# Kernel optimization log

Measured on AMD Instinct MI355X. Metric: run time of the kernel, lower is better.

The kernel has to match this reference:

```python
import jax, jax.numpy as jnp
import numpy as np

N, E, F, DE, G, C = 50000, 800000, 64, 32, 512, 2
EPS = 1e-5


def setup_inputs() -> dict:
    key = jax.random.key(0)
    ks = jax.random.split(key, 12)
    Z = 2 * F + DE  # CGConv concat dim [x_i, x_j, edge_attr]
    inp = {
        "x": jax.random.normal(ks[0], (N, F), dtype=jnp.float32),
        "edge_index": jax.random.randint(ks[1], (2, E), 0, N, dtype=jnp.int32),
        "edge_attr": jax.random.normal(ks[2], (E, DE), dtype=jnp.float32),
        "batch": jnp.sort(jax.random.randint(ks[3], (N,), 0, G, dtype=jnp.int32)),
        # CGConv lin_f / lin_s : (2F+De) -> F, with bias
        "Wf": jax.random.normal(ks[4], (Z, F), dtype=jnp.float32) * 0.05,
        "bf": jnp.zeros((F,), dtype=jnp.float32),
        "Ws": jax.random.normal(ks[5], (Z, F), dtype=jnp.float32) * 0.05,
        "bs": jnp.zeros((F,), dtype=jnp.float32),
        # CGConv internal BatchNorm (training-mode batch stats)
        "bn_w": jnp.ones((F,), dtype=jnp.float32),
        "bn_b": jnp.zeros((F,), dtype=jnp.float32),
        # PyG LayerNorm (graph mode, batch=None -> whole-tensor stats)
        "ln_w": jnp.ones((F,), dtype=jnp.float32),
        "ln_b": jnp.zeros((F,), dtype=jnp.float32),
        # final linear (2F -> C) and output LayerNorm
        "Wl": jax.random.normal(ks[6], (2 * F, C), dtype=jnp.float32) * 0.05,
        "bl": jnp.zeros((C,), dtype=jnp.float32),
        "ln4_w": jnp.ones((C,), dtype=jnp.float32),
        "ln4_b": jnp.zeros((C,), dtype=jnp.float32),
    }
    return inp


def _pyg_layernorm(x, w, b):
    # torch_geometric.nn.LayerNorm, mode='graph', batch=None: whole-tensor stats
    xc = x - jnp.mean(x)
    out = xc / (jnp.sqrt(jnp.mean(xc * xc)) + EPS)
    return out * w + b


def reference(x, edge_index, edge_attr, batch, Wf, bf, Ws, bs, bn_w, bn_b,
              ln_w, ln_b, Wl, bl, ln4_w, ln4_b):
    src = edge_index[0]  # x_j (source)
    dst = edge_index[1]  # x_i (target / aggregation index)

    # CGConv message: sigmoid(lin_f(z)) * softplus(lin_s(z)), z=[x_i,x_j,e]
    z = jnp.concatenate([x[dst], x[src], edge_attr], axis=1)  # [E, 2F+De]
    msg = jax.nn.sigmoid(z @ Wf + bf) * jax.nn.softplus(z @ Ws + bs)  # [E,F]

    # scatter-add aggregation to target nodes
    agg = jax.ops.segment_sum(msg, dst, num_segments=N)  # [N,F]

    # CGConv batch_norm=True (training-mode batch statistics over nodes)
    mu = jnp.mean(agg, axis=0)
    var = jnp.mean((agg - mu) ** 2, axis=0)
    agg = (agg - mu) / jnp.sqrt(var + EPS) * bn_w + bn_b

    # residual
    h = agg + x

    # LayerNorm + softplus
    h = jax.nn.softplus(_pyg_layernorm(h, ln_w, ln_b))

    # global mean / add pooling over graphs
    add_pool = jax.ops.segment_sum(h, batch, num_segments=G)  # [G,F]
    counts = jax.ops.segment_sum(jnp.ones((N,), h.dtype), batch, num_segments=G)
    mean_pool = add_pool / jnp.maximum(counts, 1.0)[:, None]

    g = jnp.concatenate([mean_pool, add_pool], axis=1)  # [G, 2F]
    out = g @ Wl + bl  # [G, C]
    out = _pyg_layernorm(out, ln4_w, ln4_b)
    return out
```

## Files before the change

### kernel.cpp

```cpp
#include <hip/hip_runtime.h>
#include <math.h>

#define EPSF 1e-5f

typedef short bf16x8 __attribute__((ext_vector_type(8)));
typedef float f32x4 __attribute__((ext_vector_type(4)));

static __device__ __forceinline__ unsigned short f2bf(float x) {
  unsigned u = __float_as_uint(x);
  unsigned r = (u + 0x7FFFu + ((u >> 16) & 1u)) >> 16;
  return (unsigned short)r;
}

union BU { uint4 u; bf16x8 v; };

__global__ __launch_bounds__(512) void bpack_kernel(
    const float* __restrict__ Wf, const float* __restrict__ Ws,
    unsigned short* __restrict__ Bfrag) {
  const int ks = blockIdx.x;
  const int t8 = threadIdx.x >> 6, l = threadIdx.x & 63;
  const int q = l & 15, g = l >> 4;
  const float* W = (t8 < 4) ? Wf : Ws;
  const int col = (t8 & 3) * 16 + q;
  unsigned short out[8];
#pragma unroll
  for (int i = 0; i < 8; ++i) {
    int r = ks * 32 + g * 8 + i;
    int wr = (r < 32) ? (128 + r) : (r - 32);
    out[i] = f2bf(W[(size_t)wr * 64 + col]);
  }
  *(uint4*)&Bfrag[((size_t)(ks * 8 + t8) * 64 + l) * 8] = *(uint4*)out;
}

__global__ void hist_kernel(const int* __restrict__ ei, int* __restrict__ deg,
                            int E) {
  int i = blockIdx.x * blockDim.x + threadIdx.x;
  if (i < E) atomicAdd(&deg[ei[E + i]], 1);
}

__global__ __launch_bounds__(256) void scan_a(const int* __restrict__ deg,
                                              int* __restrict__ bsum, int N) {
  const int idx = blockIdx.x * 256 + threadIdx.x;
  int v = (idx < N) ? deg[idx] : 0;
#pragma unroll
  for (int o = 32; o > 0; o >>= 1) v += __shfl_down(v, o);
  __shared__ int ws4[4];
  if ((threadIdx.x & 63) == 0) ws4[threadIdx.x >> 6] = v;
  __syncthreads();
  if (threadIdx.x == 0) bsum[blockIdx.x] = ws4[0] + ws4[1] + ws4[2] + ws4[3];
}

__global__ __launch_bounds__(256) void scan_b(const int* __restrict__ bsum,
                                              int* __restrict__ bpre, int NB) {
  const int t = threadIdx.x;
  const int lane = t & 63, w = t >> 6;
  int v = (t < NB) ? bsum[t] : 0;
  int sc = v;
#pragma unroll
  for (int o = 1; o < 64; o <<= 1) {
    int u = __shfl_up(sc, o);
    if (lane >= o) sc += u;
  }
  __shared__ int wsum[4];
  if (lane == 63) wsum[w] = sc;
  __syncthreads();
  int add = 0;
#pragma unroll
  for (int k = 0; k < 4; ++k) add += (k < w) ? wsum[k] : 0;
  bpre[t] = (sc - v) + add;
}

__global__ __launch_bounds__(256) void scan_c(const int* __restrict__ deg,
                                              const int* __restrict__ bpre,
                                              int* __restrict__ offsets,
                                              int* __restrict__ cursor, int N) {
  const int t = threadIdx.x;
  const int lane = t & 63, w = t >> 6;
  const int idx = blockIdx.x * 256 + t;
  int d = (idx < N) ? deg[idx] : 0;
  int sc = d;
#pragma unroll
  for (int o = 1; o < 64; o <<= 1) {
    int u = __shfl_up(sc, o);
    if (lane >= o) sc += u;
  }
  __shared__ int wsum[4];
  if (lane == 63) wsum[w] = sc;
  __syncthreads();
  int add = bpre[blockIdx.x];
#pragma unroll
  for (int k = 0; k < 4; ++k) add += (k < w) ? wsum[k] : 0;
  const int off = add + (sc - d);
  if (idx < N) {
    offsets[idx] = off;
    cursor[idx] = off;
    if (idx == N - 1) offsets[N] = off + d;
  }
}

__global__ void scatter_kernel(const int* __restrict__ ei,
                               int* __restrict__ cursor,
                               int4* __restrict__ epair4, int E) {
  int i = blockIdx.x * blockDim.x + threadIdx.x;
  if (i < E) {
    int dst = ei[E + i];
    int pos = atomicAdd(&cursor[dst], 1);
    epair4[pos] = make_int4(i, ei[i], dst, 0);
  }
}

__global__ __launch_bounds__(256) void edge_fused(
    const int4* __restrict__ epair4, const float* __restrict__ eattr,
    const float* __restrict__ x, const unsigned short* __restrict__ Bfrag,
    const float* __restrict__ bfv_, const float* __restrict__ bsv_,
    float* __restrict__ agg, int E, int N) {
  __shared__ __align__(16) unsigned short Ash[5][64][40];
  __shared__ __align__(16) int srcl[64];
  __shared__ __align__(16) int dstl[64];
  __shared__ __align__(16) int eidx[64];
  __shared__ __align__(4) unsigned char ridb[64];

  const int t = threadIdx.x, lane = t & 63, w = t >> 6;
  const int q = lane & 15, g = lane >> 4;
  const int base = blockIdx.x * 64;

  bf16x8 Bf[5], Bs[5];
#pragma unroll
  for (int ks = 0; ks < 5; ++ks) {
    BU u1, u2;
    u1.u = ((const uint4*)Bfrag)[(size_t)((ks * 8 + w) * 64 + lane)];
    u2.u = ((const uint4*)Bfrag)[(size_t)((ks * 8 + w + 4) * 64 + lane)];
    Bf[ks] = u1.v;
    Bs[ks] = u2.v;
  }
  const int feat = w * 16 + q;
  const float bfv = bfv_[feat];
  const float bsv = bsv_[feat];

  if (w == 0) {
    const int eg = base + lane;
    int4 p = make_int4(0, 0, 0x7FFFFFFF, 0);
    if (eg < E) p = epair4[eg];
    eidx[lane] = p.x;
    srcl[lane] = p.y;
    dstl[lane] = p.z;
    int d = p.z;
    int dprev = __shfl_up(d, 1);
    int flag = (lane == 0 || d != dprev) ? 1 : 0;
    int sc = flag;
#pragma unroll
    for (int o = 1; o < 64; o <<= 1) {
      int u = __shfl_up(sc, o);
      if (lane >= o) sc += u;
    }
    ridb[lane] = (unsigned char)(sc - 1);
  }
  __syncthreads();

  {
    const int row = t >> 2, c = t & 3;
    const int ei_ = eidx[row];
    int d_ = dstl[row];
    if (d_ >= N) d_ = 0;
    const int s_ = srcl[row];

    const float* er = eattr + (size_t)ei_ * 32 + c * 8;
    float4 v0 = *(const float4*)er;
    float4 v1 = *(const float4*)(er + 4);
    bf16x8 sv;
    sv[0] = (short)f2bf(v0.x); sv[1] = (short)f2bf(v0.y);
    sv[2] = (short)f2bf(v0.z); sv[3] = (short)f2bf(v0.w);
    sv[4] = (short)f2bf(v1.x); sv[5] = (short)f2bf(v1.y);
    sv[6] = (short)f2bf(v1.z); sv[7] = (short)f2bf(v1.w);
    *(bf16x8*)&Ash[0][row][c * 8] = sv;

    const float* xd = x + (size_t)d_ * 64 + c * 16;
    float4 a0 = *(const float4*)xd;
    float4 a1 = *(const float4*)(xd + 4);
    float4 a2 = *(const float4*)(xd + 8);
    float4 a3 = *(const float4*)(xd + 12);
    bf16x8 s0, s1;
    s0[0] = (short)f2bf(a0.x); s0[1] = (short)f2bf(a0.y);
    s0[2] = (short)f2bf(a0.z); s0[3] = (short)f2bf(a0.w);
    s0[4] = (short)f2bf(a1.x); s0[5] = (short)f2bf(a1.y);
    s0[6] = (short)f2bf(a1.z); s0[7] = (short)f2bf(a1.w);
    s1[0] = (short)f2bf(a2.x); s1[1] = (short)f2bf(a2.y);
    s1[2] = (short)f2bf(a2.z); s1[3] = (short)f2bf(a2.w);
    s1[4] = (short)f2bf(a3.x); s1[5] = (short)f2bf(a3.y);
    s1[6] = (short)f2bf(a3.z); s1[7] = (short)f2bf(a3.w);
    *(bf16x8*)&Ash[1 + (c >> 1)][row][(c & 1) * 16] = s0;
    *(bf16x8*)&Ash[1 + (c >> 1)][row][(c & 1) * 16 + 8] = s1;

    const float* xs = x + (size_t)s_ * 64 + c * 16;
    float4 b0 = *(const float4*)xs;
    float4 b1 = *(const float4*)(xs + 4);
    float4 b2 = *(const float4*)(xs + 8);
    float4 b3 = *(const float4*)(xs + 12);
    bf16x8 t0, t1;
    t0[0] = (short)f2bf(b0.x); t0[1] = (short)f2bf(b0.y);
    t0[2] = (short)f2bf(b0.z); t0[3] = (short)f2bf(b0.w);
    t0[4] = (short)f2bf(b1.x); t0[5] = (short)f2bf(b1.y);
    t0[6] = (short)f2bf(b1.z); t0[7] = (short)f2bf(b1.w);
    t1[0] = (short)f2bf(b2.x); t1[1] = (short)f2bf(b2.y);
    t1[2] = (short)f2bf(b2.z); t1[3] = (short)f2bf(b2.w);
    t1[4] = (short)f2bf(b3.x); t1[5] = (short)f2bf(b3.y);
    t1[6] = (short)f2bf(b3.z); t1[7] = (short)f2bf(b3.w);
    *(bf16x8*)&Ash[3 + (c >> 1)][row][(c & 1) * 16] = t0;
    *(bf16x8*)&Ash[3 + (c >> 1)][row][(c & 1) * 16 + 8] = t1;
  }
  __syncthreads();

  f32x4 accf[4], accs[4];
#pragma unroll
  for (int mt = 0; mt < 4; ++mt) {
    accf[mt] = (f32x4){0.f, 0.f, 0.f, 0.f};
    accs[mt] = (f32x4){0.f, 0.f, 0.f, 0.f};
  }
#pragma unroll
  for (int ks = 0; ks < 5; ++ks) {
#pragma unroll
    for (int mt = 0; mt < 4; ++mt) {
      const bf16x8 a = *(const bf16x8*)&Ash[ks][mt * 16 + q][g * 8];
      accf[mt] =
          __builtin_amdgcn_mfma_f32_16x16x32_bf16(a, Bf[ks], accf[mt], 0, 0, 0);
      accs[mt] =
          __builtin_amdgcn_mfma_f32_16x16x32_bf16(a, Bs[ks], accs[mt], 0, 0, 0);
    }
  }

#pragma unroll
  for (int mt = 0; mt < 4; ++mt) {
    const int e0 = mt * 16 + g * 4;
    const unsigned rid4 = *(const unsigned*)&ridb[e0];
    const int4 d4 = *(const int4*)&dstl[e0];
    float m[4];
#pragma unroll
    for (int r = 0; r < 4; ++r) {
      float F = accf[mt][r] + bfv;
      float S = accs[mt][r] + bsv;
      float sig = __builtin_amdgcn_rcpf(1.0f + __expf(-F));
      float sp = fmaxf(S, 0.f) + __logf(1.0f + __expf(-fabsf(S)));
      m[r] = sig * sp;
    }
    const int r0 = rid4 & 255, r1 = (rid4 >> 8) & 255, r2 = (rid4 >> 16) & 255,
              r3 = rid4 >> 24;
    float a_ = m[0];
    int cur = r0, dc = d4.x;
    if (r1 == cur) a_ += m[1];
    else {
      if (dc < N) atomicAdd(&agg[(size_t)dc * 64 + feat], a_);
      cur = r1; dc = d4.y; a_ = m[1];
    }
    if (r2 == cur) a_ += m[2];
    else {
      if (dc < N) atomicAdd(&agg[(size_t)dc * 64 + feat], a_);
      cur = r2; dc = d4.z; a_ = m[2];
    }
    if (r3 == cur) a_ += m[3];
    else {
      if (dc < N) atomicAdd(&agg[(size_t)dc * 64 + feat], a_);
      cur = r3; dc = d4.w; a_ = m[3];
    }
    if (dc < N) atomicAdd(&agg[(size_t)dc * 64 + feat], a_);
  }
}

__global__ __launch_bounds__(256) void stats_kernel(
    const float* __restrict__ agg, const float* __restrict__ x,
    float* __restrict__ stats, int N) {
  const int f = threadIdx.x & 63;
  const int sub = threadIdx.x >> 6;
  float sa = 0, sa2 = 0, sx = 0, sx2 = 0, sax = 0;
  for (int r = blockIdx.x * 4 + sub; r < N; r += gridDim.x * 4) {
    float a = agg[(size_t)r * 64 + f];
    float xv = x[(size_t)r * 64 + f];
    sa += a; sa2 += a * a; sx += xv; sx2 += xv * xv; sax += a * xv;
  }
  __shared__ float lds[4][5][64];
  lds[sub][0][f] = sa; lds[sub][1][f] = sa2; lds[sub][2][f] = sx;
  lds[sub][3][f] = sx2; lds[sub][4][f] = sax;
  __syncthreads();
  if (sub == 0) {
#pragma unroll
    for (int i = 0; i < 5; ++i) {
      float v = lds[0][i][f] + lds[1][i][f] + lds[2][i][f] + lds[3][i][f];
      atomicAdd(&stats[i * 64 + f], v);
    }
  }
}

__global__ __launch_bounds__(256) void node_finish(
    const float* __restrict__ stats, const float* __restrict__ bn_w,
    const float* __restrict__ bn_b, const float* __restrict__ agg,
    const float* __restrict__ x, const int* __restrict__ batch,
    const float* __restrict__ ln_w, const float* __restrict__ ln_b,
    float* __restrict__ add_pool, float* __restrict__ counts, int N,
    int chunk) {
  const int f = threadIdx.x & 63;
  const int sub = threadIdx.x >> 6;
  const float Nf = (float)N;
  const float invN = 1.0f / Nf;
  float Sa = stats[f], Sa2 = stats[64 + f], Sx = stats[128 + f],
        Sx2 = stats[192 + f], Sax = stats[256 + f];
  float mu = Sa * invN;
  float var = Sa2 * invN - mu * mu;
  const float alpha = bn_w[f] / sqrtf(var + EPSF);
  const float beta = bn_b[f] - mu * alpha;
  float Sh = alpha * Sa + Nf * beta + Sx;
  float Sh2 = alpha * alpha * Sa2 + Sx2 + Nf * beta * beta +
              2.f * alpha * Sax + 2.f * alpha * beta * Sa + 2.f * beta * Sx;
#pragma unroll
  for (int o = 32; o > 0; o >>= 1) {
    Sh += __shfl_xor(Sh, o);
    Sh2 += __shfl_xor(Sh2, o);
  }
  const float cnt = Nf * 64.0f;
  const float mean = Sh / cnt;
  const float msq = Sh2 / cnt - mean * mean;
  const float rden = 1.0f / (sqrtf(fmaxf(msq, 0.f)) + EPSF);
  const float lw = ln_w[f] * rden;
  const float lb = ln_b[f];

  const int r0 = blockIdx.x * chunk;
  const int r1 = min(N, r0 + chunk);
  float acc = 0.f, cacc = 0.f;
  int curg = -1;
  for (int r = r0 + sub; r < r1; r += 4) {
    int g = batch[r];
    if (g != curg) {
      if (curg >= 0) {
        atomicAdd(&add_pool[(size_t)curg * 64 + f], acc);
        if (f == 0) atomicAdd(&counts[curg], cacc);
      }
      curg = g; acc = 0.f; cacc = 0.f;
    }
    float h = fmaf(alpha, agg[(size_t)r * 64 + f], beta) + x[(size_t)r * 64 + f];
    float v = (h - mean) * lw + lb;
    float sp = fmaxf(v, 0.f) + __logf(1.0f + __expf(-fabsf(v)));
    acc += sp; cacc += 1.f;
  }
  if (curg >= 0) {
    atomicAdd(&add_pool[(size_t)curg * 64 + f], acc);
    if (f == 0) atomicAdd(&counts[curg], cacc);
  }
}

__global__ __launch_bounds__(1024) void graph_out(
    const float* __restrict__ add_pool, const float* __restrict__ counts,
    const float* __restrict__ Wl, const float* __restrict__ bl,
    const float* __restrict__ w4, const float* __restrict__ b4,
    float* __restrict__ out, int G) {
  const int t = threadIdx.x;
  const int g = t >> 1, c = t & 1;
  float cnt = fmaxf(counts[g], 1.0f);
  float inv = 1.0f / cnt;
  const float4* ap4 = (const float4*)(add_pool + (size_t)g * 64);
  const float4* W4 = (const float4*)Wl;
  float v = bl[c];
#pragma unroll 4
  for (int k4 = 0; k4 < 16; ++k4) {
    float4 a4 = ap4[k4];
    float4 wa = W4[k4 * 2];
    float4 wb = W4[k4 * 2 + 1];
    float4 wc = W4[32 + k4 * 2];
    float4 wd = W4[32 + k4 * 2 + 1];
    float m0 = c ? wa.y : wa.x, m1 = c ? wa.w : wa.z;
    float m2 = c ? wb.y : wb.x, m3 = c ? wb.w : wb.z;
    float a0 = c ? wc.y : wc.x, a1 = c ? wc.w : wc.z;
    float a2 = c ? wd.y : wd.x, a3 = c ? wd.w : wd.z;
    v = fmaf(a4.x, fmaf(m0, inv, a0), v);
    v = fmaf(a4.y, fmaf(m1, inv, a1), v);
    v = fmaf(a4.z, fmaf(m2, inv, a2), v);
    v = fmaf(a4.w, fmaf(m3, inv, a3), v);
  }

  __shared__ float red[16];
  __shared__ float bc[2];
  float sum = v;
#pragma unroll
  for (int o = 32; o > 0; o >>= 1) sum += __shfl_down(sum, o);
  if ((t & 63) == 0) red[t >> 6] = sum;
  __syncthreads();
  if (t == 0) {
    float tot = 0;
#pragma unroll
    for (int i = 0; i < 16; ++i) tot += red[i];
    bc[0] = tot * (1.0f / 1024.0f);
  }
  __syncthreads();
  const float mean = bc[0];
  const float xc = v - mean;
  float sq = xc * xc;
  __syncthreads();
#pragma unroll
  for (int o = 32; o > 0; o >>= 1) sq += __shfl_down(sq, o);
  if ((t & 63) == 0) red[t >> 6] = sq;
  __syncthreads();
  if (t == 0) {
    float tot = 0;
#pragma unroll
    for (int i = 0; i < 16; ++i) tot += red[i];
    bc[1] = 1.0f / (sqrtf(tot * (1.0f / 1024.0f)) + EPSF);
  }
  __syncthreads();
  out[t] = xc * bc[1] * w4[c] + b4[c];
}

extern "C" void kernel_launch(void* const* d_in, const int* in_sizes, int n_in,
                              void* d_out, int out_size, void* d_ws,
                              size_t ws_size, hipStream_t stream) {
  const float* x = (const float*)d_in[0];
  const int* ei = (const int*)d_in[1];
  const float* eattr = (const float*)d_in[2];
  const int* batch = (const int*)d_in[3];
  const float* Wf = (const float*)d_in[4];
  const float* bf = (const float*)d_in[5];
  const float* Ws = (const float*)d_in[6];
  const float* bs = (const float*)d_in[7];
  const float* bn_w = (const float*)d_in[8];
  const float* bn_b = (const float*)d_in[9];
  const float* ln_w = (const float*)d_in[10];
  const float* ln_b = (const float*)d_in[11];
  const float* Wl = (const float*)d_in[12];
  const float* bl = (const float*)d_in[13];
  const float* w4 = (const float*)d_in[14];
  const float* b4 = (const float*)d_in[15];

  const int N = in_sizes[0] / 64;
  const int E = in_sizes[2] / 32;
  const int G = 512;
  const int NB = (N + 255) / 256;
  const int T = (E + 63) / 64;

  float* ws = (float*)d_ws;
  float* agg = ws;
  float* stats = agg + (size_t)N * 64;
  float* add_pool = stats + 320;
  float* counts = add_pool + (size_t)G * 64;
  int* deg = (int*)(counts + G);
  int* offsets = deg + N;
  int* cursor = offsets + N + 4;
  int* bsum = cursor + N;
  int* bpre = bsum + 256;
  unsigned short* Bfrag = (unsigned short*)(bpre + 256);
  int4* epair4 = (int4*)((int*)(bpre + 256) + 10240);

  size_t zeroFloats = (size_t)N * 64 + 320 + (size_t)G * 64 + G + N;
  hipMemsetAsync(agg, 0, zeroFloats * sizeof(float), stream);

  bpack_kernel<<<5, 512, 0, stream>>>(Wf, Ws, Bfrag);
  hist_kernel<<<(E + 255) / 256, 256, 0, stream>>>(ei, deg, E);
  scan_a<<<NB, 256, 0, stream>>>(deg, bsum, N);
  scan_b<<<1, 256, 0, stream>>>(bsum, bpre, NB);
  scan_c<<<NB, 256, 0, stream>>>(deg, bpre, offsets, cursor, N);
  scatter_kernel<<<(E + 255) / 256, 256, 0, stream>>>(ei, cursor, epair4, E);
  edge_fused<<<T, 256, 0, stream>>>(epair4, eattr, x, Bfrag, bf, bs, agg, E, N);
  stats_kernel<<<512, 256, 0, stream>>>(agg, x, stats, N);
  const int chunk = (N + 511) / 512;
  node_finish<<<512, 256, 0, stream>>>(stats, bn_w, bn_b, agg, x, batch, ln_w,
                                       ln_b, add_pool, counts, N, chunk);
  graph_out<<<1, 1024, 0, stream>>>(add_pool, counts, Wl, bl, w4, b4,
                                    (float*)d_out, G);
}
```

Baseline: 334.7 us.

## Pre-convert x to bf16 and gather node rows into LDS via direct global-to-LDS loads

Adds a pre-pass kernel that converts x to bf16 once, so the edge kernel gathers half as many bytes per endpoint and no longer converts each row per edge. The x_i and x_j gathers now use global_load_lds 16-byte direct-to-LDS transfers, which skips the register round trip. The LDS row padding is removed (40 to 32 shorts) to fit the direct-load layout, which may bring back bank conflicts on the MFMA A-fragment reads. The extra conversion pass adds a small kernel and a workspace buffer.

Result: no change. 328.7 us (-1.8%).

```diff
diff --git a/kernel.cpp b/kernel.cpp
--- a/kernel.cpp
+++ b/kernel.cpp
@@ -13,6 +13,25 @@
 }
 
 union BU { uint4 u; bf16x8 v; };
+
+static __device__ __forceinline__ void gload16(const void* g, void* l) {
+  __builtin_amdgcn_global_load_lds(
+      (const __attribute__((address_space(1))) unsigned int*)g,
+      (__attribute__((address_space(3))) unsigned int*)l, 16, 0, 0);
+}
+
+__global__ __launch_bounds__(256) void cvt_x(const float* __restrict__ x,
+                                             unsigned short* __restrict__ xbf,
+                                             int total8) {
+  int i = blockIdx.x * 256 + threadIdx.x;
+  if (i >= total8) return;
+  float4 a = ((const float4*)x)[i * 2];
+  float4 b = ((const float4*)x)[i * 2 + 1];
+  unsigned short o[8];
+  o[0] = f2bf(a.x); o[1] = f2bf(a.y); o[2] = f2bf(a.z); o[3] = f2bf(a.w);
+  o[4] = f2bf(b.x); o[5] = f2bf(b.y); o[6] = f2bf(b.z); o[7] = f2bf(b.w);
+  ((uint4*)xbf)[i] = *(uint4*)o;
+}
 
 __global__ __launch_bounds__(512) void bpack_kernel(
     const float* __restrict__ Wf, const float* __restrict__ Ws,
@@ -111,10 +130,10 @@
 
 __global__ __launch_bounds__(256) void edge_fused(
     const int4* __restrict__ epair4, const float* __restrict__ eattr,
-    const float* __restrict__ x, const unsigned short* __restrict__ Bfrag,
-    const float* __restrict__ bfv_, const float* __restrict__ bsv_,
-    float* __restrict__ agg, int E, int N) {
-  __shared__ __align__(16) unsigned short Ash[5][64][40];
+    const unsigned short* __restrict__ xbf,
+    const unsigned short* __restrict__ Bfrag, const float* __restrict__ bfv_,
+    const float* __restrict__ bsv_, float* __restrict__ agg, int E, int N) {
+  __shared__ __align__(16) unsigned short Ash[5][64][32];
   __shared__ __align__(16) int srcl[64];
   __shared__ __align__(16) int dstl[64];
   __shared__ __align__(16) int eidx[64];
@@ -157,14 +176,22 @@
   }
   __syncthreads();
 
+  char* AshB = (char*)&Ash[0][0][0];
+#pragma unroll
+  for (int c2 = 0; c2 < 2; ++c2) {
+    const int k = w + c2 * 4;
+    const int row = 16 * (k & 3) + (lane >> 2);
+    const int half = (k >> 2) * 32 + (lane & 3) * 8;
+    int d = dstl[row];
+    if ((unsigned)d >= (unsigned)N) d = 0;
+    gload16(xbf + (size_t)d * 64 + half, AshB + 4096 + (size_t)k * 1024);
+    const int s = srcl[row];
+    gload16(xbf + (size_t)s * 64 + half, AshB + 12288 + (size_t)k * 1024);
+  }
+
   {
     const int row = t >> 2, c = t & 3;
-    const int ei_ = eidx[row];
-    int d_ = dstl[row];
-    if (d_ >= N) d_ = 0;
-    const int s_ = srcl[row];
-
-    const float* er = eattr + (size_t)ei_ * 32 + c * 8;
+    const float* er = eattr + (size_t)eidx[row] * 32 + c * 8;
     float4 v0 = *(const float4*)er;
     float4 v1 = *(const float4*)(er + 4);
     bf16x8 sv;
@@ -173,40 +200,6 @@
     sv[4] = (short)f2bf(v1.x); sv[5] = (short)f2bf(v1.y);
     sv[6] = (short)f2bf(v1.z); sv[7] = (short)f2bf(v1.w);
     *(bf16x8*)&Ash[0][row][c * 8] = sv;
-
-    const float* xd = x + (size_t)d_ * 64 + c * 16;
-    float4 a0 = *(const float4*)xd;
-    float4 a1 = *(const float4*)(xd + 4);
-    float4 a2 = *(const float4*)(xd + 8);
-    float4 a3 = *(const float4*)(xd + 12);
-    bf16x8 s0, s1;
-    s0[0] = (short)f2bf(a0.x); s0[1] = (short)f2bf(a0.y);
-    s0[2] = (short)f2bf(a0.z); s0[3] = (short)f2bf(a0.w);
-    s0[4] = (short)f2bf(a1.x); s0[5] = (short)f2bf(a1.y);
-    s0[6] = (short)f2bf(a1.z); s0[7] = (short)f2bf(a1.w);
-    s1[0] = (short)f2bf(a2.x); s1[1] = (short)f2bf(a2.y);
-    s1[2] = (short)f2bf(a2.z); s1[3] = (short)f2bf(a2.w);
-    s1[4] = (short)f2bf(a3.x); s1[5] = (short)f2bf(a3.y);
-    s1[6] = (short)f2bf(a3.z); s1[7] = (short)f2bf(a3.w);
-    *(bf16x8*)&Ash[1 + (c >> 1)][row][(c & 1) * 16] = s0;
-    *(bf16x8*)&Ash[1 + (c >> 1)][row][(c & 1) * 16 + 8] = s1;
-
-    const float* xs = x + (size_t)s_ * 64 + c * 16;
-    float4 b0 = *(const float4*)xs;
-    float4 b1 = *(const float4*)(xs + 4);
-    float4 b2 = *(const float4*)(xs + 8);
-    float4 b3 = *(const float4*)(xs + 12);
-    bf16x8 t0, t1;
-    t0[0] = (short)f2bf(b0.x); t0[1] = (short)f2bf(b0.y);
-    t0[2] = (short)f2bf(b0.z); t0[3] = (short)f2bf(b0.w);
-    t0[4] = (short)f2bf(b1.x); t0[5] = (short)f2bf(b1.y);
-    t0[6] = (short)f2bf(b1.z); t0[7] = (short)f2bf(b1.w);
-    t1[0] = (short)f2bf(b2.x); t1[1] = (short)f2bf(b2.y);
-    t1[2] = (short)f2bf(b2.z); t1[3] = (short)f2bf(b2.w);
-    t1[4] = (short)f2bf(b3.x); t1[5] = (short)f2bf(b3.y);
-    t1[6] = (short)f2bf(b3.z); t1[7] = (short)f2bf(b3.w);
-    *(bf16x8*)&Ash[3 + (c >> 1)][row][(c & 1) * 16] = t0;
-    *(bf16x8*)&Ash[3 + (c >> 1)][row][(c & 1) * 16 + 8] = t1;
   }
   __syncthreads();
 
@@ -443,18 +436,21 @@
   int* bsum = cursor + N;
   int* bpre = bsum + 256;
   unsigned short* Bfrag = (unsigned short*)(bpre + 256);
-  int4* epair4 = (int4*)((int*)(bpre + 256) + 10240);
+  unsigned short* xbf = Bfrag + 20480;
+  int4* epair4 = (int4*)(xbf + (size_t)N * 64);
 
   size_t zeroFloats = (size_t)N * 64 + 320 + (size_t)G * 64 + G + N;
   hipMemsetAsync(agg, 0, zeroFloats * sizeof(float), stream);
 
+  cvt_x<<<(N * 64 / 8 + 255) / 256, 256, 0, stream>>>(x, xbf, N * 64 / 8);
   bpack_kernel<<<5, 512, 0, stream>>>(Wf, Ws, Bfrag);
   hist_kernel<<<(E + 255) / 256, 256, 0, stream>>>(ei, deg, E);
   scan_a<<<NB, 256, 0, stream>>>(deg, bsum, N);
   scan_b<<<1, 256, 0, stream>>>(bsum, bpre, NB);
   scan_c<<<NB, 256, 0, stream>>>(deg, bpre, offsets, cursor, N);
   scatter_kernel<<<(E + 255) / 256, 256, 0, stream>>>(ei, cursor, epair4, E);
-  edge_fused<<<T, 256, 0, stream>>>(epair4, eattr, x, Bfrag, bf, bs, agg, E, N);
+  edge_fused<<<T, 256, 0, stream>>>(epair4, eattr, xbf, Bfrag, bf, bs, agg, E,
+                                    N);
   stats_kernel<<<512, 256, 0, stream>>>(agg, x, stats, N);
   const int chunk = (N + 511) / 512;
   node_finish<<<512, 256, 0, stream>>>(stats, bn_w, bn_b, agg, x, batch, ln_w,
```
